# Kernel optimization log

Measured on AMD Instinct MI355X. Metric: run time of the kernel, lower is better.

The kernel has to match this reference:

```python
import jax, jax.numpy as jnp
import numpy as np

N = 50000   # nodes
D = 128     # hidden_dim == in_dim
H = 4       # heads
C = 32      # hidden_dim // heads
L = 3       # message_layers
ET = 640000 # temporal edges
EH = 320000 # host edges


def layer_norm(x, g, b, eps=1e-5):
    m = x.mean(-1, keepdims=True)
    v = ((x - m) ** 2).mean(-1, keepdims=True)
    return (x - m) / jnp.sqrt(v + eps) * g + b


def transformer_conv(h, src, dst, e_emb, Wq, bq, Wk, bk, Wv, bv, We, Ws, bs):
    # PyG TransformerConv, concat=True, root_weight=True, beta=False
    n = h.shape[0]
    q = (h @ Wq + bq).reshape(n, H, C)
    k = (h @ Wk + bk).reshape(n, H, C)
    v = (h @ Wv + bv).reshape(n, H, C)
    ee = (e_emb @ We).reshape(-1, H, C)          # lin_edge has no bias
    kj = k[src] + ee                              # [E,H,C]
    a = (q[dst] * kj).sum(-1) / np.sqrt(C)        # [E,H]
    amax = jax.ops.segment_max(a, dst, num_segments=n)
    amax = jnp.where(jnp.isfinite(amax), amax, 0.0)
    ex = jnp.exp(a - amax[dst])
    den = jax.ops.segment_sum(ex, dst, num_segments=n)
    alpha = ex / (den[dst] + 1e-16)               # segment softmax over in-edges of dst
    msg = (v[src] + ee) * alpha[..., None]        # [E,H,C]
    out = jax.ops.segment_sum(msg, dst, num_segments=n).reshape(n, H * C)
    return out + h @ Ws + bs                      # root/skip connection


def mlp_head(h, W1, b1, g, bt, W2, b2):
    z = jax.nn.silu(h @ W1 + b1)
    z = layer_norm(z, g, bt)
    return z @ W2 + b2


def setup_inputs() -> dict:
    key = jax.random.key(0)
    ks = iter(jax.random.split(key, 80))
    nrm = lambda shape: jax.random.normal(next(ks), shape, jnp.float32) * 0.05
    inp = {}
    inp['x'] = jax.random.normal(next(ks), (N, D), jnp.float32)
    inp['edge_index_temporal'] = jax.random.randint(next(ks), (2, ET), 0, N)
    inp['edge_index_host'] = jax.random.randint(next(ks), (2, EH), 0, N)
    inp['edge_attr_temporal'] = jax.random.uniform(next(ks), (ET, 1), jnp.float32)
    inp['edge_attr_host'] = jax.random.normal(next(ks), (EH, 3), jnp.float32)
    # edge encoders
    inp['W_tedge'] = nrm((1, 4)); inp['b_tedge'] = jnp.zeros(4)
    inp['W_hedge'] = nrm((3, 4)); inp['b_hedge'] = jnp.zeros(4)
    # stacked conv params [L, ...] for temporal (_t) and host (_h) convs
    for s in ('t', 'h'):
        inp[f'Wq_{s}'] = nrm((L, D, D)); inp[f'bq_{s}'] = jnp.zeros((L, D))
        inp[f'Wk_{s}'] = nrm((L, D, D)); inp[f'bk_{s}'] = jnp.zeros((L, D))
        inp[f'Wv_{s}'] = nrm((L, D, D)); inp[f'bv_{s}'] = jnp.zeros((L, D))
        inp[f'We_{s}'] = nrm((L, 4, D))
        inp[f'Ws_{s}'] = nrm((L, D, D)); inp[f'bs_{s}'] = jnp.zeros((L, D))
    inp['norm_g'] = jnp.ones((L, D)); inp['norm_b'] = jnp.zeros((L, D))
    inp['fg'] = jnp.ones(D); inp['fb'] = jnp.zeros(D)
    inp['dW1'] = nrm((D, D)); inp['db1'] = jnp.zeros(D)
    inp['dg'] = jnp.ones(D); inp['dbt'] = jnp.zeros(D)
    inp['dW2'] = nrm((D, 3)); inp['db2'] = jnp.zeros(3)
    inp['sW1'] = nrm((D, D)); inp['sb1'] = jnp.zeros(D)
    inp['sg'] = jnp.ones(D); inp['sbt'] = jnp.zeros(D)
    inp['sW2'] = nrm((D, 3)); inp['sb2'] = jnp.zeros(3)
    return inp


def reference(x, edge_index_temporal, edge_index_host, edge_attr_temporal, edge_attr_host,
              W_tedge, b_tedge, W_hedge, b_hedge,
              Wq_t, bq_t, Wk_t, bk_t, Wv_t, bv_t, We_t, Ws_t, bs_t,
              Wq_h, bq_h, Wk_h, bk_h, Wv_h, bv_h, We_h, Ws_h, bs_h,
              norm_g, norm_b, fg, fb,
              dW1, db1, dg, dbt, dW2, db2,
              sW1, sb1, sg, sbt, sW2, sb2):
    te = edge_attr_temporal @ W_tedge + b_tedge   # [ET, edge_dim]
    he = edge_attr_host @ W_hedge + b_hedge       # [EH, edge_dim]
    st, dt_ = edge_index_temporal[0], edge_index_temporal[1]
    sh, dh = edge_index_host[0], edge_index_host[1]
    h = x
    for l in range(L):
        t_out = transformer_conv(h, st, dt_, te, Wq_t[l], bq_t[l], Wk_t[l], bk_t[l],
                                 Wv_t[l], bv_t[l], We_t[l], Ws_t[l], bs_t[l])
        h_out = transformer_conv(h, sh, dh, he, Wq_h[l], bq_h[l], Wk_h[l], bk_h[l],
                                 Wv_h[l], bv_h[l], We_h[l], Ws_h[l], bs_h[l])
        combined = jax.nn.silu(layer_norm(t_out + h_out, norm_g[l], norm_b[l]))
        h = h + combined  # residual (shapes match since in_dim == hidden_dim)
    h = layer_norm(h, fg, fb)
    drift = mlp_head(h, dW1, db1, dg, dbt, dW2, db2)
    diff = mlp_head(h, sW1, sb1, sg, sbt, sW2, sb2)
    return drift, diff
```

## Files before the change

kernel.cpp:

```cpp
#include <hip/hip_runtime.h>
#include <math.h>

#define NN 50000
#define DD 128
#define ET_N 640000
#define EH_N 320000
#define NL 3

static inline int cdiv(int a, int b){ return (a+b-1)/b; }

typedef __attribute__((ext_vector_type(8))) short short8;
typedef __attribute__((ext_vector_type(4))) float f32x4;

__device__ float   g_h [(size_t)NN*DD];
__device__ unsigned short g_hb[(size_t)NN*DD];
__device__ unsigned short g_Wb[(size_t)NL*8*DD*DD];
__device__ float   g_Q [2][(size_t)NN*DD];
__device__ float   g_S [2][(size_t)NN*DD];
__device__ ushort2 g_KV[2][(size_t)NN*DD];
__device__ float   g_to[(size_t)NN*DD];
__device__ float   g_ho[(size_t)NN*DD];
__device__ int     g_cnt[2][NN];
__device__ int     g_cur[2][NN];
__device__ int     g_rs [2][NN+1];
__device__ int     g_srcc[2][ET_N];
__device__ float   g_ta[ET_N];
__device__ float4  g_ha[EH_N];

__device__ inline unsigned short f2bf(float f){
  unsigned u = __float_as_uint(f);
  unsigned r = (u + 0x7fffu + ((u>>16)&1u)) >> 16;
  return (unsigned short)r;
}
__device__ inline float bf2f(unsigned short s){
  return __uint_as_float(((unsigned)s)<<16);
}
__device__ inline float bf_lo(unsigned u){ return __uint_as_float(u<<16); }
__device__ inline float bf_hi(unsigned u){ return __uint_as_float(u & 0xffff0000u); }

__global__ void k_copy_h(const float* __restrict__ x){
  int i = blockIdx.x*256 + threadIdx.x;
  if (i < NN*DD/4){
    float4 v = reinterpret_cast<const float4*>(x)[i];
    reinterpret_cast<float4*>(g_h)[i] = v;
    ushort4 b; b.x=f2bf(v.x); b.y=f2bf(v.y); b.z=f2bf(v.z); b.w=f2bf(v.w);
    reinterpret_cast<ushort4*>(g_hb)[i] = b;
  }
}

__global__ void k_zero_cnt(){
  int i = blockIdx.x*256 + threadIdx.x;
  if (i < NN) g_cnt[blockIdx.y][i] = 0;
}

struct WPtrs { const float* W[24]; };
__global__ __launch_bounds__(256) void k_cvtw(WPtrs wp){
  int mat = blockIdx.y;
  const float* W = wp.W[mat];
  int e = blockIdx.x*256 + threadIdx.x;
  int n = e >> 7, k = e & 127;
  g_Wb[(size_t)mat*DD*DD + e] = f2bf(W[k*DD+n]);
}

__global__ void k_hist(const int* __restrict__ dstT, const int* __restrict__ dstH){
  int which = blockIdx.y;
  int E = which ? EH_N : ET_N;
  const int* dst = which ? dstH : dstT;
  int e = blockIdx.x*256+threadIdx.x;
  if (e<E) atomicAdd(&g_cnt[which][dst[e]], 1);
}

__global__ __launch_bounds__(1024) void k_scan(){
  int which = blockIdx.y;
  int* row_start = g_rs[which];
  const int* cnt = g_cnt[which];
  int* cur = g_cur[which];
  __shared__ int buf[1024];
  int tid = threadIdx.x;
  const int n = NN;
  int chunk = (n + 1023) >> 10;
  int start = tid*chunk; if (start>n) start=n;
  int end = start+chunk; if (end>n) end=n;
  int lsum=0;
  for (int i=start;i<end;++i) lsum += cnt[i];
  buf[tid]=lsum;
  __syncthreads();
  for (int off=1; off<1024; off<<=1){
    int t = (tid>=off)? buf[tid-off]:0;
    __syncthreads();
    buf[tid] += t;
    __syncthreads();
  }
  int run = buf[tid]-lsum;
  for (int i=start;i<end;++i){ row_start[i]=run; cur[i]=run; run += cnt[i]; }
  if (tid==1023) row_start[n]=run;
}

__global__ void k_scatter(const int* __restrict__ eit, const int* __restrict__ eih,
                          const float* __restrict__ attrT, const float* __restrict__ attrH){
  int which = blockIdx.y;
  int e = blockIdx.x*256+threadIdx.x;
  if (which==0){
    if (e>=ET_N) return;
    int src = eit[e], dst = eit[ET_N+e];
    int p = atomicAdd(&g_cur[0][dst],1);
    g_srcc[0][p]=src;
    g_ta[p]=attrT[e];
  } else {
    if (e>=EH_N) return;
    int src = eih[e], dst = eih[EH_N+e];
    int p = atomicAdd(&g_cur[1][dst],1);
    g_srcc[1][p]=src;
    g_ha[p]=make_float4(attrH[e*3+0],attrH[e*3+1],attrH[e*3+2],0.f);
  }
}

struct BiasP { const float* b[8]; };

__global__ __launch_bounds__(256) void k_gemm_mfma(int l, BiasP bp){
  __shared__ unsigned short lA[64*DD];
  __shared__ unsigned short lB[DD*DD];
  int conv = blockIdx.y;
  int setbase = l*8 + conv*4;
  int tid = threadIdx.x;
  int m0 = blockIdx.x*64;

#pragma unroll
  for (int p=0;p<4;++p){
    int c = tid + p*256;
    int row = c >> 4, col16 = c & 15;
    int grow = m0 + row;
    uint4 v = make_uint4(0,0,0,0);
    if (grow < NN) v = *reinterpret_cast<const uint4*>(&g_hb[(size_t)grow*DD + col16*8]);
    int off = (row*256 + col16*16) ^ ((row&7)<<4);
    *reinterpret_cast<uint4*>((char*)lA + off) = v;
  }

  int wave = tid >> 6, lane = tid & 63;
  int lrow = lane & 15, kg = lane >> 4;
  int n0w = wave*32;

  auto stageB = [&](const unsigned short* Wm){
#pragma unroll
    for (int p=0;p<8;++p){
      int c = tid + p*256;
      int row = c >> 4, col16 = c & 15;
      uint4 v = *reinterpret_cast<const uint4*>(&Wm[(size_t)row*DD + col16*8]);
      int off = (row*256 + col16*16) ^ ((row&7)<<4);
      *reinterpret_cast<uint4*>((char*)lB + off) = v;
    }
  };

  stageB(&g_Wb[(size_t)(setbase+0)*DD*DD]);
  __syncthreads();

  short8 a[4][4];
#pragma unroll
  for (int kk=0;kk<4;++kk){
    int kbyte = kk*64 + kg*16;
#pragma unroll
    for (int mi=0;mi<4;++mi){
      int row = mi*16 + lrow;
      int off = (row*256 + kbyte) ^ ((row&7)<<4);
      a[kk][mi] = *reinterpret_cast<const short8*>((char*)lA + off);
    }
  }

  auto computeC = [&](f32x4 (&acc)[4][2]){
#pragma unroll
    for (int mi=0;mi<4;++mi)
#pragma unroll
      for (int ni=0;ni<2;++ni) acc[mi][ni] = (f32x4){0.f,0.f,0.f,0.f};
#pragma unroll
    for (int kk=0;kk<4;++kk){
      int kbyte = kk*64 + kg*16;
      short8 b[2];
#pragma unroll
      for (int ni=0;ni<2;++ni){
        int n = n0w + ni*16 + lrow;
        int off = (n*256 + kbyte) ^ ((n&7)<<4);
        b[ni] = *reinterpret_cast<const short8*>((char*)lB + off);
      }
#pragma unroll
      for (int mi=0;mi<4;++mi)
#pragma unroll
        for (int ni=0;ni<2;++ni)
          acc[mi][ni] = __builtin_amdgcn_mfma_f32_16x16x32_bf16(a[kk][mi], b[ni], acc[mi][ni], 0,0,0);
    }
  };

  f32x4 acc[4][2], accK[4][2];

  computeC(acc);
  {
    const float* bias = bp.b[conv*4+0];
    float* op = g_Q[conv];
#pragma unroll
    for (int ni=0;ni<2;++ni){
      int col = n0w + ni*16 + lrow;
      float bs = bias[col];
#pragma unroll
      for (int mi=0;mi<4;++mi)
#pragma unroll
        for (int r=0;r<4;++r){
          int row = m0 + mi*16 + kg*4 + r;
          if (row < NN) op[(size_t)row*DD + col] = acc[mi][ni][r] + bs;
        }
    }
  }
  __syncthreads();
  stageB(&g_Wb[(size_t)(setbase+1)*DD*DD]);
  __syncthreads();
  computeC(accK);
  __syncthreads();
  stageB(&g_Wb[(size_t)(setbase+2)*DD*DD]);
  __syncthreads();
  computeC(acc);
  {
    const float* bK = bp.b[conv*4+1];
    const float* bV = bp.b[conv*4+2];
#pragma unroll
    for (int ni=0;ni<2;++ni){
      int col = n0w + ni*16 + lrow;
      float bk = bK[col], bv = bV[col];
#pragma unroll
      for (int mi=0;mi<4;++mi)
#pragma unroll
        for (int r=0;r<4;++r){
          int row = m0 + mi*16 + kg*4 + r;
          if (row < NN){
            ushort2 kv;
            kv.x = f2bf(accK[mi][ni][r] + bk);
            kv.y = f2bf(acc [mi][ni][r] + bv);
            g_KV[conv][(size_t)row*DD + col] = kv;
          }
        }
    }
  }
  __syncthreads();
  stageB(&g_Wb[(size_t)(setbase+3)*DD*DD]);
  __syncthreads();
  computeC(acc);
  {
    const float* bias = bp.b[conv*4+3];
    float* op = g_S[conv];
#pragma unroll
    for (int ni=0;ni<2;++ni){
      int col = n0w + ni*16 + lrow;
      float bs = bias[col];
#pragma unroll
      for (int mi=0;mi<4;++mi)
#pragma unroll
        for (int r=0;r<4;++r){
          int row = m0 + mi*16 + kg*4 + r;
          if (row < NN) op[(size_t)row*DD + col] = acc[mi][ni][r] + bs;
        }
    }
  }
}

__device__ inline float waveRed(float v){
  v += __shfl_xor(v,32); v += __shfl_xor(v,16); v += __shfl_xor(v,8);
  v += __shfl_xor(v,4);  v += __shfl_xor(v,2);  v += __shfl_xor(v,1);
  return v;
}
__device__ inline float headRed16(float v){
  v += __shfl_xor(v,8); v += __shfl_xor(v,4);
  v += __shfl_xor(v,2); v += __shfl_xor(v,1);
  return v;
}

__global__ __launch_bounds__(256) void k_agg(
    const float* __restrict__ WeT, const float* __restrict__ WeH,
    const float* __restrict__ Wt,  const float* __restrict__ bt4,
    const float* __restrict__ Wh,  const float* __restrict__ bh4){
  int conv = blockIdx.y;
  int wave = threadIdx.x >> 6;
  int lane = threadIdx.x & 63;
  int i = blockIdx.x*4 + wave;
  if (i >= NN) return;
  int d0 = lane*2;

  float c0a=0.f,c1a=0.f,c2a=0.f,c3a=0.f;
  float c0b=0.f,c1b=0.f,c2b=0.f,c3b=0.f;
  if (conv==0){
#pragma unroll
    for (int j=0;j<4;++j){
      float wa=WeT[j*DD+d0], wb=WeT[j*DD+d0+1];
      c1a += Wt[j]*wa; c0a += bt4[j]*wa;
      c1b += Wt[j]*wb; c0b += bt4[j]*wb;
    }
  } else {
#pragma unroll
    for (int j=0;j<4;++j){
      float wa=WeH[j*DD+d0], wb=WeH[j*DD+d0+1];
      c0a += Wh[j]*wa; c1a += Wh[4+j]*wa; c2a += Wh[8+j]*wa; c3a += bh4[j]*wa;
      c0b += Wh[j]*wb; c1b += Wh[4+j]*wb; c2b += Wh[8+j]*wb; c3b += bh4[j]*wb;
    }
  }

  float2 q2 = *reinterpret_cast<const float2*>(&g_Q[conv][(size_t)i*DD+d0]);
  float q0 = q2.x, q1 = q2.y;
  float qe0 = headRed16(q0*c0a + q1*c0b);
  float qe1 = headRed16(q0*c1a + q1*c1b);
  float qe2=0.f, qe3=0.f;
  if (conv==1){
    qe2 = headRed16(q0*c2a + q1*c2b);
    qe3 = headRed16(q0*c3a + q1*c3b);
  }

  const int*  srcc = g_srcc[conv];
  const uint2* KV  = reinterpret_cast<const uint2*>(g_KV[conv]);
  int beg=g_rs[conv][i], end=g_rs[conv][i+1];
  int cnt = end-beg;

  const float inv32 = 0.17677669529663687f;
  float m=-INFINITY, den=0.f, ac0=0.f, ac1=0.f, x0=0.f, x1=0.f, x2=0.f;

  if (cnt>0){
    uint2 kv; float4 at=make_float4(0.f,0.f,0.f,0.f);
    {
      int s=srcc[beg];
      if (conv==0) at.x=g_ta[beg]; else at=g_ha[beg];
      kv = KV[(size_t)s*(DD/2)+lane];
    }
    for (int idx=beg; idx<end; ++idx){
      uint2 ckv=kv; float4 ca=at;
      if (idx+1<end){
        int s=srcc[idx+1];
        if (conv==0) at.x=g_ta[idx+1]; else at=g_ha[idx+1];
        kv = KV[(size_t)s*(DD/2)+lane];
      }
      float k0=bf_lo(ckv.x), v0=bf_hi(ckv.x);
      float k1=bf_lo(ckv.y), v1=bf_hi(ckv.y);
      float p = q0*k0 + q1*k1;
      p += __shfl_xor(p,8); p += __shfl_xor(p,4); p += __shfl_xor(p,2); p += __shfl_xor(p,1);
      float lg = (conv==0) ? (p + qe0 + ca.x*qe1)*inv32
                           : (p + ca.x*qe0 + ca.y*qe1 + ca.z*qe2 + qe3)*inv32;
      float nm = fmaxf(m,lg);
      float sc = __expf(m-nm);
      float ea = __expf(lg-nm);
      den = den*sc + ea;
      ac0 = ac0*sc + ea*v0;
      ac1 = ac1*sc + ea*v1;
      x0  = x0*sc + ea*ca.x;
      if (conv==1){ x1 = x1*sc + ea*ca.y; x2 = x2*sc + ea*ca.z; }
      m = nm;
    }
  }

  float r0, r1;
  if (cnt==0){
    r0 = 0.f; r1 = 0.f;
  } else {
    float id = 1.f/den;
    if (conv==0){
      float xm = x0*id;
      r0 = ac0*id + c0a + c1a*xm;
      r1 = ac1*id + c0b + c1b*xm;
    } else {
      float xm0=x0*id, xm1=x1*id, xm2=x2*id;
      r0 = ac0*id + c0a*xm0 + c1a*xm1 + c2a*xm2 + c3a;
      r1 = ac1*id + c0b*xm0 + c1b*xm1 + c2b*xm2 + c3b;
    }
  }
  float2 s2 = *reinterpret_cast<const float2*>(&g_S[conv][(size_t)i*DD+d0]);
  float* o = conv ? g_ho : g_to;
  float2 out2; out2.x = r0 + s2.x; out2.y = r1 + s2.y;
  *reinterpret_cast<float2*>(&o[(size_t)i*DD+d0]) = out2;
}

__global__ __launch_bounds__(256) void k_combine(const float* __restrict__ g, const float* __restrict__ bt){
  int lane = threadIdx.x & 63;
  int node = blockIdx.x*4 + (threadIdx.x>>6);
  if (node>=NN) return;
  size_t i0 = (size_t)node*DD + lane, i1 = i0+64;
  float v0 = g_to[i0] + g_ho[i0];
  float v1 = g_to[i1] + g_ho[i1];
  float s = waveRed(v0+v1);
  float mean = s*(1.f/128.f);
  float d0=v0-mean, d1=v1-mean;
  float q = waveRed(d0*d0+d1*d1);
  float inv = 1.f/sqrtf(q*(1.f/128.f)+1e-5f);
  float c0 = d0*inv*g[lane]+bt[lane];
  float c1 = d1*inv*g[lane+64]+bt[lane+64];
  float h0 = g_h[i0] + c0/(1.f+__expf(-c0));
  float h1 = g_h[i1] + c1/(1.f+__expf(-c1));
  g_h[i0] = h0; g_h[i1] = h1;
  g_hb[i0] = f2bf(h0); g_hb[i1] = f2bf(h1);
}

__global__ __launch_bounds__(256) void k_finalln(const float* __restrict__ g, const float* __restrict__ b){
  int lane = threadIdx.x & 63;
  int node = blockIdx.x*4 + (threadIdx.x>>6);
  if (node>=NN) return;
  size_t i0 = (size_t)node*DD + lane, i1 = i0+64;
  float v0 = g_h[i0], v1 = g_h[i1];
  float s = waveRed(v0+v1);
  float mean = s*(1.f/128.f);
  float d0=v0-mean, d1=v1-mean;
  float q = waveRed(d0*d0+d1*d1);
  float inv = 1.f/sqrtf(q*(1.f/128.f)+1e-5f);
  g_h[i0]=d0*inv*g[lane]+b[lane];
  g_h[i1]=d1*inv*g[lane+64]+b[lane+64];
}

__global__ __launch_bounds__(128) void k_head(
      const float* __restrict__ W1, const float* __restrict__ b1,
      const float* __restrict__ g, const float* __restrict__ bt,
      const float* __restrict__ W2, const float* __restrict__ b2,
      float* __restrict__ out){
  int d = threadIdx.x;
  int wv = d >> 6;
  int i0 = blockIdx.x*8;
  const int n = NN;
  __shared__ float rows[8][DD];
  __shared__ float comb[2];
#pragma unroll
  for (int t=0;t<8;++t){
    int node = i0+t;
    rows[t][d] = (node<n)? g_h[(size_t)node*DD+d] : 0.f;
  }
  __syncthreads();
  float z[8];
  float b1d = b1[d];
#pragma unroll
  for (int t=0;t<8;++t) z[t]=b1d;
  for (int k=0;k<DD;++k){
    float w = W1[k*DD+d];
#pragma unroll
    for (int t=0;t<8;++t) z[t] += rows[t][k]*w;
  }
#pragma unroll
  for (int t=0;t<8;++t){ float v=z[t]; z[t] = v/(1.f+expf(-v)); }
  float gd=g[d], btd=bt[d];
  float w2a=W2[d*3+0], w2b=W2[d*3+1], w2c=W2[d*3+2];
  float b2a=b2[0], b2b=b2[1], b2c=b2[2];
  for (int t=0;t<8;++t){
    int node=i0+t;
    float zz=z[t];
    float s = waveRed(zz);
    if ((d&63)==0) comb[wv]=s;
    __syncthreads();
    float mean=(comb[0]+comb[1])*(1.f/128.f);
    __syncthreads();
    float dv=zz-mean;
    float q2 = waveRed(dv*dv);
    if ((d&63)==0) comb[wv]=q2;
    __syncthreads();
    float inv = 1.f/sqrtf((comb[0]+comb[1])*(1.f/128.f)+1e-5f);
    __syncthreads();
    float zn = dv*inv*gd+btd;
    float p0 = waveRed(zn*w2a);
    if ((d&63)==0) comb[wv]=p0;
    __syncthreads();
    float o0 = comb[0]+comb[1]+b2a;
    __syncthreads();
    float p1 = waveRed(zn*w2b);
    if ((d&63)==0) comb[wv]=p1;
    __syncthreads();
    float o1 = comb[0]+comb[1]+b2b;
    __syncthreads();
    float p2 = waveRed(zn*w2c);
    if ((d&63)==0) comb[wv]=p2;
    __syncthreads();
    float o2 = comb[0]+comb[1]+b2c;
    __syncthreads();
    if (d==0 && node<n){
      out[(size_t)node*3+0]=o0; out[(size_t)node*3+1]=o1; out[(size_t)node*3+2]=o2;
    }
  }
}

extern "C" void kernel_launch(void* const* d_in, const int* in_sizes, int n_in,
                              void* d_out, int out_size, void* d_ws, size_t ws_size,
                              hipStream_t stream){
  (void)in_sizes; (void)n_in; (void)out_size; (void)d_ws; (void)ws_size;
  const float* x    = (const float*)d_in[0];
  const int*   eit  = (const int*)d_in[1];
  const int*   eih  = (const int*)d_in[2];
  const float* eat  = (const float*)d_in[3];
  const float* eah  = (const float*)d_in[4];
  const float* W_te = (const float*)d_in[5];
  const float* b_te = (const float*)d_in[6];
  const float* W_he = (const float*)d_in[7];
  const float* b_he = (const float*)d_in[8];
  const float *Wq_t=(const float*)d_in[9],  *bq_t=(const float*)d_in[10];
  const float *Wk_t=(const float*)d_in[11], *bk_t=(const float*)d_in[12];
  const float *Wv_t=(const float*)d_in[13], *bv_t=(const float*)d_in[14];
  const float *We_t=(const float*)d_in[15];
  const float *Ws_t=(const float*)d_in[16], *bs_t=(const float*)d_in[17];
  const float *Wq_h=(const float*)d_in[18], *bq_h=(const float*)d_in[19];
  const float *Wk_h=(const float*)d_in[20], *bk_h=(const float*)d_in[21];
  const float *Wv_h=(const float*)d_in[22], *bv_h=(const float*)d_in[23];
  const float *We_h=(const float*)d_in[24];
  const float *Ws_h=(const float*)d_in[25], *bs_h=(const float*)d_in[26];
  const float *norm_g=(const float*)d_in[27], *norm_b=(const float*)d_in[28];
  const float *fg=(const float*)d_in[29], *fb=(const float*)d_in[30];
  const float *dW1=(const float*)d_in[31], *db1=(const float*)d_in[32];
  const float *dg=(const float*)d_in[33],  *dbt=(const float*)d_in[34];
  const float *dW2=(const float*)d_in[35], *db2=(const float*)d_in[36];
  const float *sW1=(const float*)d_in[37], *sb1=(const float*)d_in[38];
  const float *sg=(const float*)d_in[39],  *sbt=(const float*)d_in[40];
  const float *sW2=(const float*)d_in[41], *sb2=(const float*)d_in[42];
  float* outp = (float*)d_out;

  k_copy_h<<<cdiv(NN*DD/4,256),256,0,stream>>>(x);

  WPtrs wp;
  for (int l=0;l<NL;++l){
    wp.W[l*8+0]=Wq_t+(size_t)l*DD*DD; wp.W[l*8+1]=Wk_t+(size_t)l*DD*DD;
    wp.W[l*8+2]=Wv_t+(size_t)l*DD*DD; wp.W[l*8+3]=Ws_t+(size_t)l*DD*DD;
    wp.W[l*8+4]=Wq_h+(size_t)l*DD*DD; wp.W[l*8+5]=Wk_h+(size_t)l*DD*DD;
    wp.W[l*8+6]=Wv_h+(size_t)l*DD*DD; wp.W[l*8+7]=Ws_h+(size_t)l*DD*DD;
  }
  k_cvtw<<<dim3(64,24),256,0,stream>>>(wp);

  k_zero_cnt<<<dim3(cdiv(NN,256),2),256,0,stream>>>();
  k_hist<<<dim3(cdiv(ET_N,256),2),256,0,stream>>>(eit+ET_N, eih+EH_N);
  k_scan<<<dim3(1,2),1024,0,stream>>>();
  k_scatter<<<dim3(cdiv(ET_N,256),2),256,0,stream>>>(eit, eih, eat, eah);

  for (int l=0;l<NL;++l){
    BiasP bp;
    bp.b[0]=bq_t+(size_t)l*DD; bp.b[1]=bk_t+(size_t)l*DD;
    bp.b[2]=bv_t+(size_t)l*DD; bp.b[3]=bs_t+(size_t)l*DD;
    bp.b[4]=bq_h+(size_t)l*DD; bp.b[5]=bk_h+(size_t)l*DD;
    bp.b[6]=bv_h+(size_t)l*DD; bp.b[7]=bs_h+(size_t)l*DD;
    k_gemm_mfma<<<dim3(cdiv(NN,64),2),256,0,stream>>>(l, bp);
    k_agg<<<dim3(cdiv(NN,4),2),256,0,stream>>>(We_t+(size_t)l*4*DD, We_h+(size_t)l*4*DD,
                                               W_te, b_te, W_he, b_he);
    k_combine<<<cdiv(NN,4),256,0,stream>>>(norm_g+(size_t)l*DD, norm_b+(size_t)l*DD);
  }
  k_finalln<<<cdiv(NN,4),256,0,stream>>>(fg, fb);
  k_head<<<cdiv(NN,8),128,0,stream>>>(dW1, db1, dg, dbt, dW2, db2, outp);
  k_head<<<cdiv(NN,8),128,0,stream>>>(sW1, sb1, sg, sbt, sW2, sb2, outp+(size_t)NN*3);
}
```

Baseline: 1.224 ms.

## Process four edges per wave in aggregation and drop online-max softmax

The edge aggregation kernel is rewritten so each wave splits into four 16-lane groups. Each group handles a different in-edge at the same time, and each lane loads 8 channels of packed bf16 K/V with 128-bit loads. Per-group partial sums are combined with cross-group shuffles at the end. The running-max rescaling of the online softmax is removed and exp(logit) is accumulated directly. This saves exponentials and serial dependencies and adds memory-level parallelism, but it can overflow if logits become large.

Result: no change. 1.241 ms (+1.3%).

```diff
diff --git a/kernel.cpp b/kernel.cpp
--- a/kernel.cpp
+++ b/kernel.cpp
@@ -264,11 +264,6 @@
   v += __shfl_xor(v,4);  v += __shfl_xor(v,2);  v += __shfl_xor(v,1);
   return v;
 }
-__device__ inline float headRed16(float v){
-  v += __shfl_xor(v,8); v += __shfl_xor(v,4);
-  v += __shfl_xor(v,2); v += __shfl_xor(v,1);
-  return v;
-}
 
 __global__ __launch_bounds__(256) void k_agg(
     const float* __restrict__ WeT, const float* __restrict__ WeH,
@@ -279,95 +274,146 @@
   int lane = threadIdx.x & 63;
   int i = blockIdx.x*4 + wave;
   if (i >= NN) return;
-  int d0 = lane*2;
-
-  float c0a=0.f,c1a=0.f,c2a=0.f,c3a=0.f;
-  float c0b=0.f,c1b=0.f,c2b=0.f,c3b=0.f;
+  int g = lane >> 4;
+  int t = lane & 15;
+  int ch0 = t*8;
+
+  const float* Qi = &g_Q[conv][(size_t)i*DD + ch0];
+  float q[8];
+  {
+    float4 qA = *reinterpret_cast<const float4*>(Qi);
+    float4 qB = *reinterpret_cast<const float4*>(Qi+4);
+    q[0]=qA.x;q[1]=qA.y;q[2]=qA.z;q[3]=qA.w;q[4]=qB.x;q[5]=qB.y;q[6]=qB.z;q[7]=qB.w;
+  }
+
+  float cB[8], cA0[8], cA1[8], cA2[8];
+#pragma unroll
+  for (int r=0;r<8;++r){ cB[r]=0.f; cA0[r]=0.f; cA1[r]=0.f; cA2[r]=0.f; }
   if (conv==0){
 #pragma unroll
     for (int j=0;j<4;++j){
-      float wa=WeT[j*DD+d0], wb=WeT[j*DD+d0+1];
-      c1a += Wt[j]*wa; c0a += bt4[j]*wa;
-      c1b += Wt[j]*wb; c0b += bt4[j]*wb;
+      float4 wA = *reinterpret_cast<const float4*>(&WeT[j*DD+ch0]);
+      float4 wB = *reinterpret_cast<const float4*>(&WeT[j*DD+ch0+4]);
+      float w[8]={wA.x,wA.y,wA.z,wA.w,wB.x,wB.y,wB.z,wB.w};
+      float bj=bt4[j], aj=Wt[j];
+#pragma unroll
+      for (int r=0;r<8;++r){ cB[r] += bj*w[r]; cA0[r] += aj*w[r]; }
     }
   } else {
 #pragma unroll
     for (int j=0;j<4;++j){
-      float wa=WeH[j*DD+d0], wb=WeH[j*DD+d0+1];
-      c0a += Wh[j]*wa; c1a += Wh[4+j]*wa; c2a += Wh[8+j]*wa; c3a += bh4[j]*wa;
-      c0b += Wh[j]*wb; c1b += Wh[4+j]*wb; c2b += Wh[8+j]*wb; c3b += bh4[j]*wb;
-    }
-  }
-
-  float2 q2 = *reinterpret_cast<const float2*>(&g_Q[conv][(size_t)i*DD+d0]);
-  float q0 = q2.x, q1 = q2.y;
-  float qe0 = headRed16(q0*c0a + q1*c0b);
-  float qe1 = headRed16(q0*c1a + q1*c1b);
-  float qe2=0.f, qe3=0.f;
+      float4 wA = *reinterpret_cast<const float4*>(&WeH[j*DD+ch0]);
+      float4 wB = *reinterpret_cast<const float4*>(&WeH[j*DD+ch0+4]);
+      float w[8]={wA.x,wA.y,wA.z,wA.w,wB.x,wB.y,wB.z,wB.w};
+      float a0=Wh[j], a1=Wh[4+j], a2=Wh[8+j], bj=bh4[j];
+#pragma unroll
+      for (int r=0;r<8;++r){ cA0[r]+=a0*w[r]; cA1[r]+=a1*w[r]; cA2[r]+=a2*w[r]; cB[r]+=bj*w[r]; }
+    }
+  }
+
+  float qeB=0.f, qe0=0.f, qe1=0.f, qe2=0.f;
+#pragma unroll
+  for (int r=0;r<8;++r){ qeB += q[r]*cB[r]; qe0 += q[r]*cA0[r]; }
+  qeB += __shfl_xor(qeB,1); qeB += __shfl_xor(qeB,2);
+  qe0 += __shfl_xor(qe0,1); qe0 += __shfl_xor(qe0,2);
   if (conv==1){
-    qe2 = headRed16(q0*c2a + q1*c2b);
-    qe3 = headRed16(q0*c3a + q1*c3b);
-  }
-
-  const int*  srcc = g_srcc[conv];
-  const uint2* KV  = reinterpret_cast<const uint2*>(g_KV[conv]);
+#pragma unroll
+    for (int r=0;r<8;++r){ qe1 += q[r]*cA1[r]; qe2 += q[r]*cA2[r]; }
+    qe1 += __shfl_xor(qe1,1); qe1 += __shfl_xor(qe1,2);
+    qe2 += __shfl_xor(qe2,1); qe2 += __shfl_xor(qe2,2);
+  }
+
+  const int* srcc = g_srcc[conv];
+  const char* KVbase = (const char*)g_KV[conv];
   int beg=g_rs[conv][i], end=g_rs[conv][i+1];
   int cnt = end-beg;
 
   const float inv32 = 0.17677669529663687f;
-  float m=-INFINITY, den=0.f, ac0=0.f, ac1=0.f, x0=0.f, x1=0.f, x2=0.f;
+  float den=0.f, x0=0.f, x1=0.f, x2=0.f;
+  float ac[8];
+#pragma unroll
+  for (int r=0;r<8;++r) ac[r]=0.f;
 
   if (cnt>0){
-    uint2 kv; float4 at=make_float4(0.f,0.f,0.f,0.f);
-    {
-      int s=srcc[beg];
-      if (conv==0) at.x=g_ta[beg]; else at=g_ha[beg];
-      kv = KV[(size_t)s*(DD/2)+lane];
-    }
-    for (int idx=beg; idx<end; ++idx){
-      uint2 ckv=kv; float4 ca=at;
-      if (idx+1<end){
-        int s=srcc[idx+1];
-        if (conv==0) at.x=g_ta[idx+1]; else at=g_ha[idx+1];
-        kv = KV[(size_t)s*(DD/2)+lane];
+    int nit = (cnt+3)>>2;
+    int idx = beg + g;
+    bool val = idx < end;
+    int sidx = val ? idx : beg;
+    int s = srcc[sidx];
+    float4 at = make_float4(0.f,0.f,0.f,0.f);
+    if (conv==0) at.x = g_ta[sidx]; else at = g_ha[sidx];
+    const uint4* rp = reinterpret_cast<const uint4*>(KVbase + (size_t)s*512 + t*32);
+    uint4 u0 = rp[0], u1 = rp[1];
+
+    for (int it=0; it<nit; ++it){
+      uint4 cu0=u0, cu1=u1; float4 ca=at; bool cval=val;
+      if (it+1<nit){
+        int nidx = beg + (it+1)*4 + g;
+        val = nidx < end;
+        int ns = srcc[val?nidx:beg];
+        if (conv==0) at.x = g_ta[val?nidx:beg]; else at = g_ha[val?nidx:beg];
+        rp = reinterpret_cast<const uint4*>(KVbase + (size_t)ns*512 + t*32);
+        u0 = rp[0]; u1 = rp[1];
       }
-      float k0=bf_lo(ckv.x), v0=bf_hi(ckv.x);
-      float k1=bf_lo(ckv.y), v1=bf_hi(ckv.y);
-      float p = q0*k0 + q1*k1;
-      p += __shfl_xor(p,8); p += __shfl_xor(p,4); p += __shfl_xor(p,2); p += __shfl_xor(p,1);
-      float lg = (conv==0) ? (p + qe0 + ca.x*qe1)*inv32
-                           : (p + ca.x*qe0 + ca.y*qe1 + ca.z*qe2 + qe3)*inv32;
-      float nm = fmaxf(m,lg);
-      float sc = __expf(m-nm);
-      float ea = __expf(lg-nm);
-      den = den*sc + ea;
-      ac0 = ac0*sc + ea*v0;
-      ac1 = ac1*sc + ea*v1;
-      x0  = x0*sc + ea*ca.x;
-      if (conv==1){ x1 = x1*sc + ea*ca.y; x2 = x2*sc + ea*ca.z; }
-      m = nm;
-    }
-  }
-
-  float r0, r1;
-  if (cnt==0){
-    r0 = 0.f; r1 = 0.f;
-  } else {
-    float id = 1.f/den;
-    if (conv==0){
-      float xm = x0*id;
-      r0 = ac0*id + c0a + c1a*xm;
-      r1 = ac1*id + c0b + c1b*xm;
+      float k[8], v[8];
+      k[0]=bf_lo(cu0.x); v[0]=bf_hi(cu0.x);
+      k[1]=bf_lo(cu0.y); v[1]=bf_hi(cu0.y);
+      k[2]=bf_lo(cu0.z); v[2]=bf_hi(cu0.z);
+      k[3]=bf_lo(cu0.w); v[3]=bf_hi(cu0.w);
+      k[4]=bf_lo(cu1.x); v[4]=bf_hi(cu1.x);
+      k[5]=bf_lo(cu1.y); v[5]=bf_hi(cu1.y);
+      k[6]=bf_lo(cu1.z); v[6]=bf_hi(cu1.z);
+      k[7]=bf_lo(cu1.w); v[7]=bf_hi(cu1.w);
+      float p = 0.f;
+#pragma unroll
+      for (int r=0;r<8;++r) p += q[r]*k[r];
+      p += __shfl_xor(p,1); p += __shfl_xor(p,2);
+      float lg = (conv==0) ? (p + qeB + ca.x*qe0)*inv32
+                           : (p + ca.x*qe0 + ca.y*qe1 + ca.z*qe2 + qeB)*inv32;
+      float e = cval ? __expf(lg) : 0.f;
+      den += e;
+#pragma unroll
+      for (int r=0;r<8;++r) ac[r] += e*v[r];
+      x0 += e*ca.x;
+      if (conv==1){ x1 += e*ca.y; x2 += e*ca.z; }
+    }
+    den += __shfl_xor(den,16); den += __shfl_xor(den,32);
+    x0  += __shfl_xor(x0,16);  x0  += __shfl_xor(x0,32);
+    if (conv==1){
+      x1 += __shfl_xor(x1,16); x1 += __shfl_xor(x1,32);
+      x2 += __shfl_xor(x2,16); x2 += __shfl_xor(x2,32);
+    }
+#pragma unroll
+    for (int r=0;r<8;++r){ ac[r] += __shfl_xor(ac[r],16); ac[r] += __shfl_xor(ac[r],32); }
+  }
+
+  if (g==0){
+    float r8[8];
+    if (cnt==0){
+#pragma unroll
+      for (int r=0;r<8;++r) r8[r]=0.f;
     } else {
-      float xm0=x0*id, xm1=x1*id, xm2=x2*id;
-      r0 = ac0*id + c0a*xm0 + c1a*xm1 + c2a*xm2 + c3a;
-      r1 = ac1*id + c0b*xm0 + c1b*xm1 + c2b*xm2 + c3b;
-    }
-  }
-  float2 s2 = *reinterpret_cast<const float2*>(&g_S[conv][(size_t)i*DD+d0]);
-  float* o = conv ? g_ho : g_to;
-  float2 out2; out2.x = r0 + s2.x; out2.y = r1 + s2.y;
-  *reinterpret_cast<float2*>(&o[(size_t)i*DD+d0]) = out2;
+      float id = 1.f/den;
+      if (conv==0){
+        float xm = x0*id;
+#pragma unroll
+        for (int r=0;r<8;++r) r8[r] = ac[r]*id + cB[r] + cA0[r]*xm;
+      } else {
+        float xm0=x0*id, xm1=x1*id, xm2=x2*id;
+#pragma unroll
+        for (int r=0;r<8;++r) r8[r] = ac[r]*id + cA0[r]*xm0 + cA1[r]*xm1 + cA2[r]*xm2 + cB[r];
+      }
+    }
+    const float* Si = &g_S[conv][(size_t)i*DD + ch0];
+    float4 sA = *reinterpret_cast<const float4*>(Si);
+    float4 sB = *reinterpret_cast<const float4*>(Si+4);
+    float* o = (conv ? g_ho : g_to) + (size_t)i*DD + ch0;
+    float4 oA, oB;
+    oA.x=r8[0]+sA.x; oA.y=r8[1]+sA.y; oA.z=r8[2]+sA.z; oA.w=r8[3]+sA.w;
+    oB.x=r8[4]+sB.x; oB.y=r8[5]+sB.y; oB.z=r8[6]+sB.z; oB.w=r8[7]+sB.w;
+    *reinterpret_cast<float4*>(o)   = oA;
+    *reinterpret_cast<float4*>(o+4) = oB;
+  }
 }
 
 __global__ __launch_bounds__(256) void k_combine(const float* __restrict__ g, const float* __restrict__ bt){
```
